# Kernel tuning notes

Hardware: AMD Instinct MI355X
Metric: run time of the kernel (lower is better)

The kernel has to match this reference:

```python
import jax, jax.numpy as jnp
import numpy as np
import math

B, C, H, W = 8, 96, 256, 256
WS = 8            # window_size
NH = 3            # num_heads
HD = C // NH      # head_dim = 32


def setup_inputs() -> dict:
    key = jax.random.key(0)
    ks = jax.random.split(key, 8)
    f = lambda k, s: jax.random.normal(k, s, dtype=jnp.float32) * 0.02
    return {
        "X": jax.random.normal(ks[0], (B, C, H, W), dtype=jnp.float32),
        "Wq": f(ks[1], (C, C)), "bq": jnp.zeros((C,), jnp.float32),
        "Wkv": f(ks[2], (2 * C, C)), "bkv": jnp.zeros((2 * C,), jnp.float32),
        "dw_w": f(ks[3], (C, 1, 5, 5)), "dw_b": jnp.zeros((C,), jnp.float32),
        "Wproj": f(ks[4], (C, C)), "bproj": jnp.zeros((C,), jnp.float32),
        "logit_scale": jnp.array(math.log(1.0 / 0.07), jnp.float32),
        "meta_w1": f(ks[5], (256, 2)), "meta_b1": jnp.zeros((256,), jnp.float32),
        "meta_w2": f(ks[6], (NH, 256)), "meta_b2": jnp.zeros((NH,), jnp.float32),
    }


def _rel_pos_log():
    # get_relative_positions(WS): [N, N, 2] with sign(d)*log(1+|d|)
    coords = jnp.stack(jnp.meshgrid(jnp.arange(WS), jnp.arange(WS), indexing='ij'))
    coords = coords.reshape(2, -1)                      # [2, N]
    rel = (coords[:, :, None] - coords[:, None, :]).transpose(1, 2, 0).astype(jnp.float32)
    return jnp.sign(rel) * jnp.log1p(jnp.abs(rel))      # [N, N, 2]


def _window_partition(x):
    # x: [B, c, H, W] -> [nW, WS*WS, c]
    c = x.shape[1]
    x = x.transpose(0, 2, 3, 1).reshape(B, H // WS, WS, W // WS, WS, c)
    return x.transpose(0, 1, 3, 2, 4, 5).reshape(-1, WS * WS, c)


def reference(X, Wq, bq, Wkv, bkv, dw_w, dw_b, Wproj, bproj,
              logit_scale, meta_w1, meta_b1, meta_w2, meta_b2):
    # 1x1 convs as channel matmuls
    Q = jnp.einsum('bchw,oc->bohw', X, Wq) + bq[None, :, None, None]
    KV = jnp.einsum('bchw,oc->bohw', X, Wkv) + bkv[None, :, None, None]
    QKV = jnp.concatenate([Q, KV], axis=1)              # [B, 3C, H, W]

    # depthwise 5x5 conv with reflect padding on Q
    Qp = jnp.pad(Q, ((0, 0), (0, 0), (2, 2), (2, 2)), mode='reflect')
    conv_out = jax.lax.conv_general_dilated(
        Qp, dw_w, window_strides=(1, 1), padding='VALID',
        feature_group_count=C,
        dimension_numbers=('NCHW', 'OIHW', 'NCHW')) + dw_b[None, :, None, None]

    # window partition (shift_size=0, H/W divisible by WS -> check_size is identity)
    qkv = _window_partition(QKV)                        # [nW, N, 3C]
    co = _window_partition(conv_out)                    # [nW, N, C]
    N = WS * WS
    nW = qkv.shape[0]

    qkv = qkv.reshape(nW, N, 3, NH, HD).transpose(2, 0, 3, 1, 4)  # [3, nW, NH, N, HD]
    q = co.reshape(nW, N, NH, HD).transpose(0, 2, 1, 3)           # conv query path
    k = qkv[1] * (HD ** -0.5)
    v = qkv[2]

    ls = jnp.exp(jnp.minimum(logit_scale, math.log(100.0)))
    attn = jnp.einsum('whnd,whmd->whnm', q, k) * ls     # [nW, NH, N, N]

    # MLP relative position bias
    rel = _rel_pos_log()                                # [N, N, 2]
    bias = jax.nn.relu(rel @ meta_w1.T + meta_b1) @ meta_w2.T + meta_b2  # [N, N, NH]
    attn = attn + bias.transpose(2, 0, 1)[None]
    attn = jax.nn.softmax(attn, axis=-1)

    x = jnp.einsum('whnm,whmd->whnd', attn, v)          # [nW, NH, N, HD]
    x = x.transpose(0, 2, 1, 3).reshape(nW, N, C)

    # window reverse -> [B, H, W, C] -> NCHW
    x = x.reshape(B, H // WS, W // WS, WS, WS, C).transpose(0, 1, 3, 2, 4, 5)
    x = x.reshape(B, H, W, C).transpose(0, 3, 1, 2)

    return jnp.einsum('bchw,oc->bohw', x, Wproj) + bproj[None, :, None, None]
```

## Files before the change

### kernel.cpp

```cpp
#include <hip/hip_runtime.h>
#include <math.h>

#define HW 65536

__global__ __launch_bounds__(256) void bias_mlp_kernel(
    const float* __restrict__ w1, const float* __restrict__ b1,
    const float* __restrict__ w2, const float* __restrict__ b2,
    float* __restrict__ biasT)
{
    int id = blockIdx.x * 256 + threadIdx.x;
    int i = id >> 6, j = id & 63;
    float dy = (float)((i >> 3) - (j >> 3));
    float dx = (float)((i & 7) - (j & 7));
    float r0 = copysignf(log1pf(fabsf(dy)), dy);
    float r1 = copysignf(log1pf(fabsf(dx)), dx);
    float a0 = b2[0], a1 = b2[1], a2 = b2[2];
    for (int m = 0; m < 256; ++m) {
        float h = fmaf(r0, w1[2*m], fmaf(r1, w1[2*m+1], b1[m]));
        h = fmaxf(h, 0.f);
        a0 = fmaf(h, w2[m],       a0);
        a1 = fmaf(h, w2[256 + m], a1);
        a2 = fmaf(h, w2[512 + m], a2);
    }
    biasT[(0*64 + j)*64 + i] = a0;
    biasT[(1*64 + j)*64 + i] = a1;
    biasT[(2*64 + j)*64 + i] = a2;
}

__global__ __launch_bounds__(256) void gemm1x1_kernel(
    const float* __restrict__ X,
    const float* __restrict__ W0,  const float* __restrict__ W12,
    const float* __restrict__ bias0, const float* __restrict__ bias12,
    const float* __restrict__ lsptr,
    float* __restrict__ out0, float* __restrict__ out1, float* __restrict__ out2)
{
    const int tid = threadIdx.x;
    const int z = blockIdx.y;
    int t = (blockIdx.x & 7) * (gridDim.x >> 3) + (blockIdx.x >> 3);
    const int b    = t >> 9;
    const int pos0 = (t & 511) << 7;

    const float* Wmat = (z == 0) ? W0     : (z == 1 ? W12    : W12 + 96*96);
    const float* bias = (z == 0) ? bias0  : (z == 1 ? bias12 : bias12 + 96);
    float*       out  = (z == 0) ? out0   : (z == 1 ? out1   : out2);
    float scale = 1.0f;
    if (z == 1)
        scale = __expf(fminf(lsptr[0], 4.6051702f)) * 0.17677669529663687f;

    __shared__ float Xs[32][128];
    __shared__ float Ws[32][96];

    const int tx = tid & 31, ty = tid >> 5;
    float acc[12][4];
    #pragma unroll
    for (int u = 0; u < 12; ++u)
        #pragma unroll
        for (int p = 0; p < 4; ++p) acc[u][p] = 0.f;

    const float* Xb = X + (size_t)b * 96 * HW + pos0;

    for (int kc = 0; kc < 96; kc += 32) {
        #pragma unroll
        for (int jj = 0; jj < 4; ++jj) {
            int i4 = tid + jj*256;
            int kr = i4 >> 5, p4 = i4 & 31;
            float4 v = *reinterpret_cast<const float4*>(Xb + (size_t)(kc + kr)*HW + p4*4);
            *reinterpret_cast<float4*>(&Xs[kr][p4*4]) = v;
        }
        #pragma unroll
        for (int jj = 0; jj < 3; ++jj) {
            int i4 = tid + jj*256;
            int o = i4 >> 3, c4 = i4 & 7;
            float4 v = *reinterpret_cast<const float4*>(Wmat + o*96 + kc + c4*4);
            Ws[c4*4+0][o] = v.x; Ws[c4*4+1][o] = v.y;
            Ws[c4*4+2][o] = v.z; Ws[c4*4+3][o] = v.w;
        }
        __syncthreads();
        #pragma unroll 8
        for (int k = 0; k < 32; ++k) {
            float4 xr = *reinterpret_cast<const float4*>(&Xs[k][tx*4]);
            float4 wa = *reinterpret_cast<const float4*>(&Ws[k][ty*12]);
            float4 wb = *reinterpret_cast<const float4*>(&Ws[k][ty*12+4]);
            float4 wc = *reinterpret_cast<const float4*>(&Ws[k][ty*12+8]);
            float wv[12] = {wa.x,wa.y,wa.z,wa.w, wb.x,wb.y,wb.z,wb.w, wc.x,wc.y,wc.z,wc.w};
            float xv[4]  = {xr.x, xr.y, xr.z, xr.w};
            #pragma unroll
            for (int u = 0; u < 12; ++u)
                #pragma unroll
                for (int p = 0; p < 4; ++p)
                    acc[u][p] = fmaf(wv[u], xv[p], acc[u][p]);
        }
        __syncthreads();
    }

    float* ob = out + (size_t)b * 96 * HW + pos0 + tx*4;
    #pragma unroll
    for (int u = 0; u < 12; ++u) {
        int o = ty*12 + u;
        float bv = bias[o];
        float4 r;
        r.x = (acc[u][0] + bv) * scale;
        r.y = (acc[u][1] + bv) * scale;
        r.z = (acc[u][2] + bv) * scale;
        r.w = (acc[u][3] + bv) * scale;
        *reinterpret_cast<float4*>(ob + (size_t)o * HW) = r;
    }
}

__global__ __launch_bounds__(256) void dwconv5x5_kernel(
    const float* __restrict__ Q, const float* __restrict__ dw,
    const float* __restrict__ db, float* __restrict__ out)
{
    int bid = (blockIdx.x & 7) * (gridDim.x >> 3) + (blockIdx.x >> 3);
    const int bc = bid >> 5;
    const int h0 = (bid & 31) << 3;
    const int c  = bc % 96;
    const int tid = threadIdx.x;

    __shared__ float t[12][264];

    const float* Qb = Q + (size_t)bc * HW;
    #pragma unroll
    for (int jj = 0; jj < 3; ++jj) {
        int i4 = tid + jj*256;
        int r = i4 >> 6, c4 = i4 & 63;
        int imr = h0 - 2 + r;
        imr = imr < 0 ? -imr : (imr > 255 ? 510 - imr : imr);
        float4 v = *reinterpret_cast<const float4*>(Qb + imr*256 + c4*4);
        *reinterpret_cast<float4*>(&t[r][4 + c4*4]) = v;
    }
    if (tid < 48) {
        int r = tid >> 2, which = tid & 3;
        int imr = h0 - 2 + r;
        imr = imr < 0 ? -imr : (imr > 255 ? 510 - imr : imr);
        int L  = (which < 2) ? (2 + which) : (258 + which);
        int gc = (which == 0) ? 2 : (which == 1) ? 1 : (which == 2) ? 254 : 253;
        t[r][L] = Qb[imr*256 + gc];
    }
    __syncthreads();

    float w[25];
    #pragma unroll
    for (int q = 0; q < 25; ++q) w[q] = dw[c*25 + q];
    const float bv = db[c];

    float accv[8];
    #pragma unroll
    for (int r = 0; r < 8; ++r) accv[r] = bv;

    #pragma unroll
    for (int kx = 0; kx < 5; ++kx) {
        float col[12];
        #pragma unroll
        for (int rr = 0; rr < 12; ++rr) col[rr] = t[rr][tid + kx + 2];
        #pragma unroll
        for (int r = 0; r < 8; ++r)
            #pragma unroll
            for (int ky = 0; ky < 5; ++ky)
                accv[r] = fmaf(w[ky*5 + kx], col[r + ky], accv[r]);
    }

    float* ob = out + (size_t)bc * HW + h0*256 + tid;
    #pragma unroll
    for (int r = 0; r < 8; ++r)
        ob[r*256] = accv[r];
}

__global__ __launch_bounds__(192, 2) void winattn_kernel(
    const float* __restrict__ q, const float* __restrict__ K,
    const float* __restrict__ V, const float* __restrict__ biasT,
    float* __restrict__ out)
{
    int t = (blockIdx.x & 7) * (gridDim.x >> 3) + (blockIdx.x >> 3);
    const int b = t >> 10, wy = (t >> 5) & 31, wx = t & 31;
    const int tid  = threadIdx.x;
    const int head = tid >> 6, lane = tid & 63;

    __shared__ float Kl[64][100];
    __shared__ float Vl[64][100];

    const size_t wbase = ((size_t)b * 96 * 256 + (size_t)wy * 8) * 256 + wx * 8;

    for (int i = tid; i < 6144; i += 192) {
        int cc = i >> 6, p = i & 63;
        size_t g = wbase + (size_t)cc * HW + (size_t)(p >> 3) * 256 + (p & 7);
        Kl[p][cc] = K[g];
        Vl[p][cc] = V[g];
    }

    const int py = lane >> 3, px = lane & 7;
    const size_t qbase = wbase + (size_t)head * 32 * HW + py * 256 + px;
    float qr[32];
    #pragma unroll
    for (int d = 0; d < 32; ++d) qr[d] = q[qbase + (size_t)d * HW];

    __syncthreads();

    float acc[32];
    #pragma unroll
    for (int d = 0; d < 32; ++d) acc[d] = 0.f;
    float sum = 0.f;

    const float* bT = biasT + head * 4096 + lane;
    #pragma unroll 4
    for (int j = 0; j < 64; ++j) {
        const float4* kr = reinterpret_cast<const float4*>(&Kl[j][head*32]);
        float dot = bT[j*64];
        #pragma unroll
        for (int d4 = 0; d4 < 8; ++d4) {
            float4 kv = kr[d4];
            dot = fmaf(qr[d4*4+0], kv.x, dot);
            dot = fmaf(qr[d4*4+1], kv.y, dot);
            dot = fmaf(qr[d4*4+2], kv.z, dot);
            dot = fmaf(qr[d4*4+3], kv.w, dot);
        }
        float p = __expf(dot);
        sum += p;
        const float4* vr = reinterpret_cast<const float4*>(&Vl[j][head*32]);
        #pragma unroll
        for (int d4 = 0; d4 < 8; ++d4) {
            float4 vv = vr[d4];
            acc[d4*4+0] = fmaf(p, vv.x, acc[d4*4+0]);
            acc[d4*4+1] = fmaf(p, vv.y, acc[d4*4+1]);
            acc[d4*4+2] = fmaf(p, vv.z, acc[d4*4+2]);
            acc[d4*4+3] = fmaf(p, vv.w, acc[d4*4+3]);
        }
    }

    const float inv = 1.0f / sum;
    #pragma unroll
    for (int d = 0; d < 32; ++d)
        out[qbase + (size_t)d * HW] = acc[d] * inv;
}

extern "C" void kernel_launch(void* const* d_in, const int* in_sizes, int n_in,
                              void* d_out, int out_size, void* d_ws, size_t ws_size,
                              hipStream_t stream)
{
    const float* X     = (const float*)d_in[0];
    const float* Wq    = (const float*)d_in[1];
    const float* bq    = (const float*)d_in[2];
    const float* Wkv   = (const float*)d_in[3];
    const float* bkv   = (const float*)d_in[4];
    const float* dww   = (const float*)d_in[5];
    const float* dwb   = (const float*)d_in[6];
    const float* Wproj = (const float*)d_in[7];
    const float* bproj = (const float*)d_in[8];
    const float* ls    = (const float*)d_in[9];
    const float* mw1   = (const float*)d_in[10];
    const float* mb1   = (const float*)d_in[11];
    const float* mw2   = (const float*)d_in[12];
    const float* mb2   = (const float*)d_in[13];
    float* out = (float*)d_out;

    const size_t perBatch = (size_t)96 * HW;
    int nb = 8;
    while (nb > 1 &&
           (12288 + (size_t)3 * nb * perBatch) * sizeof(float) > ws_size)
        nb >>= 1;

    float* biasT = (float*)d_ws;
    float* f0 = biasT + 12288;
    float* f1 = f0 + (size_t)nb * perBatch;
    float* f2 = f1 + (size_t)nb * perBatch;

    bias_mlp_kernel<<<16, 256, 0, stream>>>(mw1, mb1, mw2, mb2, biasT);

    for (int b0 = 0; b0 < 8; b0 += nb) {
        const float* Xc  = X   + (size_t)b0 * perBatch;
        float*       oc  = out + (size_t)b0 * perBatch;
        gemm1x1_kernel<<<dim3(512 * nb, 3), 256, 0, stream>>>(
            Xc, Wq, Wkv, bq, bkv, ls, f0, f1, f2);
        dwconv5x5_kernel<<<3072 * nb, 256, 0, stream>>>(f0, dww, dwb, oc);
        winattn_kernel<<<1024 * nb, 192, 0, stream>>>(oc, f1, f2, biasT, f0);
        gemm1x1_kernel<<<dim3(512 * nb, 1), 256, 0, stream>>>(
            f0, Wproj, Wkv, bproj, bkv, ls, oc, f1, f2);
    }
}
```

Baseline: 1.259 ms.

## Use bf16 MFMA for QKV and projection GEMMs with window-major bf16 K/V intermediates

The fp32 FMA 1x1-conv GEMMs are replaced by bf16 MFMA kernels: one fused QKV kernel and one projection kernel. K, V and the attention output are now stored as bf16 in a window-major layout, so the attention and projection kernels can load them contiguously with 16-byte loads, and the write/read traffic for these intermediates is halved. Attention uses bf16 fdot2 for QK when available. The cost is reduced precision in the K/V/attention intermediates and in the GEMM inputs, which may push numerical error close to the tolerance.

```diff
diff --git a/kernel.cpp b/kernel.cpp
--- a/kernel.cpp
+++ b/kernel.cpp
@@ -2,6 +2,24 @@
 #include <math.h>
 
 #define HW 65536
+typedef unsigned short u16;
+typedef unsigned int   u32;
+typedef __bf16 bf16_t;
+typedef bf16_t bf16x8 __attribute__((ext_vector_type(8)));
+typedef bf16_t bf16x2 __attribute__((ext_vector_type(2)));
+typedef float  f32x4  __attribute__((ext_vector_type(4)));
+
+#if defined(__has_builtin)
+#if __has_builtin(__builtin_amdgcn_fdot2_f32_bf16)
+#define HAS_FDOT2 1
+#endif
+#endif
+
+__device__ __forceinline__ u16 f2bf(float x) {
+    return __builtin_bit_cast(u16, (bf16_t)x);
+}
+__device__ __forceinline__ float bflo(u32 d) { return __uint_as_float(d << 16); }
+__device__ __forceinline__ float bfhi(u32 d) { return __uint_as_float(d & 0xffff0000u); }
 
 __global__ __launch_bounds__(256) void bias_mlp_kernel(
     const float* __restrict__ w1, const float* __restrict__ b1,
@@ -27,83 +45,103 @@
     biasT[(2*64 + j)*64 + i] = a2;
 }
 
-__global__ __launch_bounds__(256) void gemm1x1_kernel(
-    const float* __restrict__ X,
-    const float* __restrict__ W0,  const float* __restrict__ W12,
-    const float* __restrict__ bias0, const float* __restrict__ bias12,
-    const float* __restrict__ lsptr,
-    float* __restrict__ out0, float* __restrict__ out1, float* __restrict__ out2)
+__global__ __launch_bounds__(384) void qkv_mfma_kernel(
+    const float* __restrict__ X,  const float* __restrict__ Wq,
+    const float* __restrict__ bq, const float* __restrict__ Wkv,
+    const float* __restrict__ bkv, const float* __restrict__ lsptr,
+    float* __restrict__ Qout, u16* __restrict__ Kw, u16* __restrict__ Vw)
 {
     const int tid = threadIdx.x;
-    const int z = blockIdx.y;
-    int t = (blockIdx.x & 7) * (gridDim.x >> 3) + (blockIdx.x >> 3);
+    int t = ((blockIdx.x & 7) * (gridDim.x >> 3)) + (blockIdx.x >> 3);
     const int b    = t >> 9;
-    const int pos0 = (t & 511) << 7;
-
-    const float* Wmat = (z == 0) ? W0     : (z == 1 ? W12    : W12 + 96*96);
-    const float* bias = (z == 0) ? bias0  : (z == 1 ? bias12 : bias12 + 96);
-    float*       out  = (z == 0) ? out0   : (z == 1 ? out1   : out2);
-    float scale = 1.0f;
-    if (z == 1)
-        scale = __expf(fminf(lsptr[0], 4.6051702f)) * 0.17677669529663687f;
-
-    __shared__ float Xs[32][128];
-    __shared__ float Ws[32][96];
-
-    const int tx = tid & 31, ty = tid >> 5;
-    float acc[12][4];
-    #pragma unroll
-    for (int u = 0; u < 12; ++u)
-        #pragma unroll
-        for (int p = 0; p < 4; ++p) acc[u][p] = 0.f;
-
-    const float* Xb = X + (size_t)b * 96 * HW + pos0;
-
-    for (int kc = 0; kc < 96; kc += 32) {
-        #pragma unroll
-        for (int jj = 0; jj < 4; ++jj) {
-            int i4 = tid + jj*256;
-            int kr = i4 >> 5, p4 = i4 & 31;
-            float4 v = *reinterpret_cast<const float4*>(Xb + (size_t)(kc + kr)*HW + p4*4);
-            *reinterpret_cast<float4*>(&Xs[kr][p4*4]) = v;
-        }
-        #pragma unroll
-        for (int jj = 0; jj < 3; ++jj) {
-            int i4 = tid + jj*256;
-            int o = i4 >> 3, c4 = i4 & 7;
-            float4 v = *reinterpret_cast<const float4*>(Wmat + o*96 + kc + c4*4);
-            Ws[c4*4+0][o] = v.x; Ws[c4*4+1][o] = v.y;
-            Ws[c4*4+2][o] = v.z; Ws[c4*4+3][o] = v.w;
-        }
-        __syncthreads();
-        #pragma unroll 8
-        for (int k = 0; k < 32; ++k) {
-            float4 xr = *reinterpret_cast<const float4*>(&Xs[k][tx*4]);
-            float4 wa = *reinterpret_cast<const float4*>(&Ws[k][ty*12]);
-            float4 wb = *reinterpret_cast<const float4*>(&Ws[k][ty*12+4]);
-            float4 wc = *reinterpret_cast<const float4*>(&Ws[k][ty*12+8]);
-            float wv[12] = {wa.x,wa.y,wa.z,wa.w, wb.x,wb.y,wb.z,wb.w, wc.x,wc.y,wc.z,wc.w};
-            float xv[4]  = {xr.x, xr.y, xr.z, xr.w};
+    const int tile = t & 511;
+    const int band = tile >> 4;
+    const int wcol = tile & 15;
+
+    __shared__ u16 Xs[128][104];
+
+    const float* Xb = X + (size_t)band * 8 * 256 + wcol * 16 + (size_t)b * 96 * HW;
+
+    #pragma unroll
+    for (int j = 0; j < 8; ++j) {
+        int i4 = tid + j * 384;
+        int k  = i4 >> 5;
+        int rr = (i4 >> 2) & 7;
+        int c4 = (i4 & 3) * 4;
+        float4 v = *reinterpret_cast<const float4*>(Xb + (size_t)k * HW + rr * 256 + c4);
+        int n = rr * 16 + c4;
+        Xs[n+0][k] = f2bf(v.x);
+        Xs[n+1][k] = f2bf(v.y);
+        Xs[n+2][k] = f2bf(v.z);
+        Xs[n+3][k] = f2bf(v.w);
+    }
+    __syncthreads();
+
+    const int wave = tid >> 6, l = tid & 63;
+    const int m0 = wave * 48;
+    const int lrow = l & 15, lq = l >> 4;
+
+    f32x4 acc[3][8];
+    #pragma unroll
+    for (int mt = 0; mt < 3; ++mt)
+        #pragma unroll
+        for (int nt = 0; nt < 8; ++nt)
+            acc[mt][nt] = (f32x4){0.f, 0.f, 0.f, 0.f};
+
+    #pragma unroll
+    for (int ks = 0; ks < 3; ++ks) {
+        const int k0 = ks * 32 + lq * 8;
+        bf16x8 afr[3];
+        #pragma unroll
+        for (int mt = 0; mt < 3; ++mt) {
+            int m = m0 + mt * 16 + lrow;
+            const float* Wrow = (m < 96) ? (Wq + m * 96) : (Wkv + (m - 96) * 96);
+            float4 wa = *reinterpret_cast<const float4*>(Wrow + k0);
+            float4 wb = *reinterpret_cast<const float4*>(Wrow + k0 + 4);
+            bf16x8 af;
+            af[0] = (bf16_t)wa.x; af[1] = (bf16_t)wa.y;
+            af[2] = (bf16_t)wa.z; af[3] = (bf16_t)wa.w;
+            af[4] = (bf16_t)wb.x; af[5] = (bf16_t)wb.y;
+            af[6] = (bf16_t)wb.z; af[7] = (bf16_t)wb.w;
+            afr[mt] = af;
+        }
+        #pragma unroll
+        for (int nt = 0; nt < 8; ++nt) {
+            bf16x8 bf = *reinterpret_cast<const bf16x8*>(&Xs[nt * 16 + lrow][k0]);
             #pragma unroll
-            for (int u = 0; u < 12; ++u)
-                #pragma unroll
-                for (int p = 0; p < 4; ++p)
-                    acc[u][p] = fmaf(wv[u], xv[p], acc[u][p]);
-        }
-        __syncthreads();
-    }
-
-    float* ob = out + (size_t)b * 96 * HW + pos0 + tx*4;
-    #pragma unroll
-    for (int u = 0; u < 12; ++u) {
-        int o = ty*12 + u;
-        float bv = bias[o];
-        float4 r;
-        r.x = (acc[u][0] + bv) * scale;
-        r.y = (acc[u][1] + bv) * scale;
-        r.z = (acc[u][2] + bv) * scale;
-        r.w = (acc[u][3] + bv) * scale;
-        *reinterpret_cast<float4*>(ob + (size_t)o * HW) = r;
+            for (int mt = 0; mt < 3; ++mt)
+                acc[mt][nt] = __builtin_amdgcn_mfma_f32_16x16x32_bf16(
+                    afr[mt], bf, acc[mt][nt], 0, 0, 0);
+        }
+    }
+
+    const float s = __expf(fminf(lsptr[0], 4.6051702f)) * 0.17677669529663687f;
+
+    #pragma unroll
+    for (int mt = 0; mt < 3; ++mt) {
+        #pragma unroll
+        for (int nt = 0; nt < 8; ++nt) {
+            #pragma unroll
+            for (int r = 0; r < 4; ++r) {
+                float v = acc[mt][nt][r];
+                int o = m0 + mt * 16 + lq * 4 + r;
+                if (o < 96) {
+                    Qout[(size_t)b * 96 * HW + (size_t)o * HW +
+                         (band * 8 + nt) * 256 + wcol * 16 + lrow] = v + bq[o];
+                } else {
+                    int win = band * 32 + wcol * 2 + (lrow >> 3);
+                    int wpos = nt * 8 + (lrow & 7);
+                    size_t idx = ((size_t)(b * 1024 + win) * 64 + wpos) * 96;
+                    if (o < 192) {
+                        int ch = o - 96;
+                        Kw[idx + ch] = f2bf((v + bkv[ch]) * s);
+                    } else {
+                        int ch = o - 192;
+                        Vw[idx + ch] = f2bf(v + bkv[96 + ch]);
+                    }
+                }
+            }
+        }
     }
 }
 
@@ -166,35 +204,46 @@
         ob[r*256] = accv[r];
 }
 
-__global__ __launch_bounds__(192, 2) void winattn_kernel(
-    const float* __restrict__ q, const float* __restrict__ K,
-    const float* __restrict__ V, const float* __restrict__ biasT,
-    float* __restrict__ out)
+__global__ __launch_bounds__(192) void winattn_kernel(
+    const float* __restrict__ q, const u16* __restrict__ Kw,
+    const u16* __restrict__ Vw, const float* __restrict__ biasT,
+    u16* __restrict__ Ow)
 {
     int t = (blockIdx.x & 7) * (gridDim.x >> 3) + (blockIdx.x >> 3);
-    const int b = t >> 10, wy = (t >> 5) & 31, wx = t & 31;
+    const int b = t >> 10, win = t & 1023;
     const int tid  = threadIdx.x;
     const int head = tid >> 6, lane = tid & 63;
 
-    __shared__ float Kl[64][100];
-    __shared__ float Vl[64][100];
-
-    const size_t wbase = ((size_t)b * 96 * 256 + (size_t)wy * 8) * 256 + wx * 8;
-
-    for (int i = tid; i < 6144; i += 192) {
-        int cc = i >> 6, p = i & 63;
-        size_t g = wbase + (size_t)cc * HW + (size_t)(p >> 3) * 256 + (p & 7);
-        Kl[p][cc] = K[g];
-        Vl[p][cc] = V[g];
-    }
-
+    __shared__ u16 Kl[64][104];
+    __shared__ u16 Vl[64][104];
+
+    const int wy = win >> 5, wx = win & 31;
     const int py = lane >> 3, px = lane & 7;
-    const size_t qbase = wbase + (size_t)head * 32 * HW + py * 256 + px;
+    const size_t qbase = (size_t)b * 96 * HW + (size_t)head * 32 * HW +
+                         (size_t)(wy * 8 + py) * 256 + wx * 8 + px;
     float qr[32];
     #pragma unroll
     for (int d = 0; d < 32; ++d) qr[d] = q[qbase + (size_t)d * HW];
 
+    const uint4* Kg = reinterpret_cast<const uint4*>(Kw + (size_t)(b * 1024 + win) * 6144);
+    const uint4* Vg = reinterpret_cast<const uint4*>(Vw + (size_t)(b * 1024 + win) * 6144);
+    #pragma unroll
+    for (int j = 0; j < 4; ++j) {
+        int i4 = tid + j * 192;
+        int n = i4 / 12, c8 = i4 % 12;
+        *reinterpret_cast<uint4*>(&Kl[n][c8 * 8]) = Kg[i4];
+        *reinterpret_cast<uint4*>(&Vl[n][c8 * 8]) = Vg[i4];
+    }
     __syncthreads();
+
+#ifdef HAS_FDOT2
+    bf16x2 qp[16];
+    #pragma unroll
+    for (int i = 0; i < 16; ++i) {
+        bf16x2 p; p[0] = (bf16_t)qr[2*i]; p[1] = (bf16_t)qr[2*i+1];
+        qp[i] = p;
+    }
+#endif
 
     float acc[32];
     #pragma unroll
@@ -204,33 +253,130 @@
     const float* bT = biasT + head * 4096 + lane;
     #pragma unroll 4
     for (int j = 0; j < 64; ++j) {
-        const float4* kr = reinterpret_cast<const float4*>(&Kl[j][head*32]);
-        float dot = bT[j*64];
-        #pragma unroll
-        for (int d4 = 0; d4 < 8; ++d4) {
-            float4 kv = kr[d4];
-            dot = fmaf(qr[d4*4+0], kv.x, dot);
-            dot = fmaf(qr[d4*4+1], kv.y, dot);
-            dot = fmaf(qr[d4*4+2], kv.z, dot);
-            dot = fmaf(qr[d4*4+3], kv.w, dot);
-        }
+        const uint4* kr = reinterpret_cast<const uint4*>(&Kl[j][head * 32]);
+        uint4 ka = kr[0], kb = kr[1], kc = kr[2], kd = kr[3];
+        float dot = bT[j * 64];
+#ifdef HAS_FDOT2
+        u32 kw[16] = {ka.x,ka.y,ka.z,ka.w, kb.x,kb.y,kb.z,kb.w,
+                      kc.x,kc.y,kc.z,kc.w, kd.x,kd.y,kd.z,kd.w};
+        #pragma unroll
+        for (int i = 0; i < 16; ++i)
+            dot = __builtin_amdgcn_fdot2_f32_bf16(
+                qp[i], __builtin_bit_cast(bf16x2, kw[i]), dot, false);
+#else
+        u32 kw[16] = {ka.x,ka.y,ka.z,ka.w, kb.x,kb.y,kb.z,kb.w,
+                      kc.x,kc.y,kc.z,kc.w, kd.x,kd.y,kd.z,kd.w};
+        #pragma unroll
+        for (int i = 0; i < 16; ++i) {
+            dot = fmaf(qr[2*i],   bflo(kw[i]), dot);
+            dot = fmaf(qr[2*i+1], bfhi(kw[i]), dot);
+        }
+#endif
         float p = __expf(dot);
         sum += p;
-        const float4* vr = reinterpret_cast<const float4*>(&Vl[j][head*32]);
-        #pragma unroll
-        for (int d4 = 0; d4 < 8; ++d4) {
-            float4 vv = vr[d4];
-            acc[d4*4+0] = fmaf(p, vv.x, acc[d4*4+0]);
-            acc[d4*4+1] = fmaf(p, vv.y, acc[d4*4+1]);
-            acc[d4*4+2] = fmaf(p, vv.z, acc[d4*4+2]);
-            acc[d4*4+3] = fmaf(p, vv.w, acc[d4*4+3]);
+        const uint4* vr = reinterpret_cast<const uint4*>(&Vl[j][head * 32]);
+        uint4 va = vr[0], vb = vr[1], vc = vr[2], vd = vr[3];
+        u32 vw[16] = {va.x,va.y,va.z,va.w, vb.x,vb.y,vb.z,vb.w,
+                      vc.x,vc.y,vc.z,vc.w, vd.x,vd.y,vd.z,vd.w};
+        #pragma unroll
+        for (int i = 0; i < 16; ++i) {
+            acc[2*i]   = fmaf(p, bflo(vw[i]), acc[2*i]);
+            acc[2*i+1] = fmaf(p, bfhi(vw[i]), acc[2*i+1]);
         }
     }
 
     const float inv = 1.0f / sum;
-    #pragma unroll
-    for (int d = 0; d < 32; ++d)
-        out[qbase + (size_t)d * HW] = acc[d] * inv;
+    u32 ow[16];
+    #pragma unroll
+    for (int i = 0; i < 16; ++i) {
+        u32 lo = f2bf(acc[2*i]   * inv);
+        u32 hi = f2bf(acc[2*i+1] * inv);
+        ow[i] = lo | (hi << 16);
+    }
+    uint4* ob = reinterpret_cast<uint4*>(
+        Ow + ((size_t)(b * 1024 + win) * 64 + lane) * 96 + head * 32);
+    ob[0] = (uint4){ow[0],  ow[1],  ow[2],  ow[3]};
+    ob[1] = (uint4){ow[4],  ow[5],  ow[6],  ow[7]};
+    ob[2] = (uint4){ow[8],  ow[9],  ow[10], ow[11]};
+    ob[3] = (uint4){ow[12], ow[13], ow[14], ow[15]};
+}
+
+__global__ __launch_bounds__(192) void proj_mfma_kernel(
+    const u16* __restrict__ Aw, const float* __restrict__ Wproj,
+    const float* __restrict__ bproj, float* __restrict__ out)
+{
+    const int tid = threadIdx.x;
+    int t = ((blockIdx.x & 7) * (gridDim.x >> 3)) + (blockIdx.x >> 3);
+    const int b    = t >> 9;
+    const int tile = t & 511;
+    const int band = tile >> 4;
+    const int wp   = tile & 15;
+
+    __shared__ u16 Xs[128][104];
+
+    const uint4* Ag = reinterpret_cast<const uint4*>(
+        Aw + (size_t)(b * 1024 + band * 32 + wp * 2) * 6144);
+    #pragma unroll
+    for (int j = 0; j < 8; ++j) {
+        int i4 = tid + j * 192;
+        int n = i4 / 12, c8 = i4 % 12;
+        *reinterpret_cast<uint4*>(&Xs[n][c8 * 8]) = Ag[i4];
+    }
+    __syncthreads();
+
+    const int wave = tid >> 6, l = tid & 63;
+    const int m0 = wave * 32;
+    const int lrow = l & 15, lq = l >> 4;
+
+    f32x4 acc[2][8];
+    #pragma unroll
+    for (int mt = 0; mt < 2; ++mt)
+        #pragma unroll
+        for (int nt = 0; nt < 8; ++nt)
+            acc[mt][nt] = (f32x4){0.f, 0.f, 0.f, 0.f};
+
+    #pragma unroll
+    for (int ks = 0; ks < 3; ++ks) {
+        const int k0 = ks * 32 + lq * 8;
+        bf16x8 afr[2];
+        #pragma unroll
+        for (int mt = 0; mt < 2; ++mt) {
+            const float* Wrow = Wproj + (m0 + mt * 16 + lrow) * 96;
+            float4 wa = *reinterpret_cast<const float4*>(Wrow + k0);
+            float4 wb = *reinterpret_cast<const float4*>(Wrow + k0 + 4);
+            bf16x8 af;
+            af[0] = (bf16_t)wa.x; af[1] = (bf16_t)wa.y;
+            af[2] = (bf16_t)wa.z; af[3] = (bf16_t)wa.w;
+            af[4] = (bf16_t)wb.x; af[5] = (bf16_t)wb.y;
+            af[6] = (bf16_t)wb.z; af[7] = (bf16_t)wb.w;
+            afr[mt] = af;
+        }
+        #pragma unroll
+        for (int nt = 0; nt < 8; ++nt) {
+            bf16x8 bf = *reinterpret_cast<const bf16x8*>(&Xs[nt * 16 + lrow][k0]);
+            #pragma unroll
+            for (int mt = 0; mt < 2; ++mt)
+                acc[mt][nt] = __builtin_amdgcn_mfma_f32_16x16x32_bf16(
+                    afr[mt], bf, acc[mt][nt], 0, 0, 0);
+        }
+    }
+
+    #pragma unroll
+    for (int mt = 0; mt < 2; ++mt) {
+        #pragma unroll
+        for (int nt = 0; nt < 8; ++nt) {
+            #pragma unroll
+            for (int r = 0; r < 4; ++r) {
+                int o = m0 + mt * 16 + lq * 4 + r;
+                int n = nt * 16 + lrow;
+                int wl = n >> 6, wpos = n & 63;
+                int h = band * 8 + (wpos >> 3);
+                int wimg = wp * 16 + wl * 8 + (wpos & 7);
+                out[(size_t)b * 96 * HW + (size_t)o * HW + h * 256 + wimg] =
+                    acc[mt][nt][r] + bproj[o];
+            }
+        }
+    }
 }
 
 extern "C" void kernel_launch(void* const* d_in, const int* in_sizes, int n_in,
@@ -256,24 +402,25 @@
     const size_t perBatch = (size_t)96 * HW;
     int nb = 8;
     while (nb > 1 &&
-           (12288 + (size_t)3 * nb * perBatch) * sizeof(float) > ws_size)
+           49152 + (size_t)nb * perBatch * 8 > ws_size)
         nb >>= 1;
 
     float* biasT = (float*)d_ws;
-    float* f0 = biasT + 12288;
-    float* f1 = f0 + (size_t)nb * perBatch;
-    float* f2 = f1 + (size_t)nb * perBatch;
+    float* f0    = biasT + 12288;
+    u16*   Kw    = (u16*)(f0 + (size_t)nb * perBatch);
+    u16*   Vw    = Kw + (size_t)nb * perBatch;
 
     bias_mlp_kernel<<<16, 256, 0, stream>>>(mw1, mb1, mw2, mb2, biasT);
 
     for (int b0 = 0; b0 < 8; b0 += nb) {
-        const float* Xc  = X   + (size_t)b0 * perBatch;
-        float*       oc  = out + (size_t)b0 * perBatch;
-        gemm1x1_kernel<<<dim3(512 * nb, 3), 256, 0, stream>>>(
-            Xc, Wq, Wkv, bq, bkv, ls, f0, f1, f2);
+        const float* Xc = X   + (size_t)b0 * perBatch;
+        float*       oc = out + (size_t)b0 * perBatch;
+        qkv_mfma_kernel<<<512 * nb, 384, 0, stream>>>(
+            Xc, Wq, bq, Wkv, bkv, ls, f0, Kw, Vw);
         dwconv5x5_kernel<<<3072 * nb, 256, 0, stream>>>(f0, dww, dwb, oc);
-        winattn_kernel<<<1024 * nb, 192, 0, stream>>>(oc, f1, f2, biasT, f0);
-        gemm1x1_kernel<<<dim3(512 * nb, 1), 256, 0, stream>>>(
-            f0, Wproj, Wkv, bproj, bkv, ls, oc, f1, f2);
-    }
-}
+        winattn_kernel<<<1024 * nb, 192, 0, stream>>>(
+            oc, Kw, Vw, biasT, (u16*)f0);
+        proj_mfma_kernel<<<512 * nb, 192, 0, stream>>>(
+            (u16*)f0, Wproj, bproj, oc);
+    }
+}
```

Result: no change. 1.275 ms (+1.3%).
